# Kernel tuning notes

Hardware: AMD Instinct MI355X
Metric: run time of the kernel (lower is better)

The kernel has to match this reference:

```python
import jax, jax.numpy as jnp
import numpy as np

B, S, D, M = 2, 4096, 128, 64

def _linear_init(key, shape, fan_in):
    bound = 1.0 / np.sqrt(fan_in)
    return jax.random.uniform(key, shape, jnp.float32, -bound, bound)

def setup_inputs() -> dict:
    key = jax.random.key(0)
    ks = jax.random.split(key, 18)
    x = jax.random.normal(ks[0], (B, S, D), jnp.float32)
    context = jax.random.normal(ks[1], (B, S, D), jnp.float32)
    # per-mechanism params (torch Linear semantics: y = x @ W.T + b)
    Wt = _linear_init(ks[2], (M, D, D), D)   # transform weight, laid out [m, in, out]
    bt = _linear_init(ks[3], (M, D), D)
    char = jax.random.normal(ks[4], (M, D), jnp.float32)  # characteristics [1,1,d] per mech
    Wg = _linear_init(ks[5], (M, D), D)      # timing_gate weight (out=1)
    bg = _linear_init(ks[6], (M,), D)
    Wv = _linear_init(ks[7], (M, D), D)      # victory_detector weight (out=1)
    bv = _linear_init(ks[8], (M,), D)
    O = jax.random.normal(ks[9], (M, M), jnp.float32) * 0.02  # overcoming matrix
    # selector: Linear(2D,2D) -> GELU -> Linear(2D,M)
    W1 = _linear_init(ks[10], (2 * D, 2 * D), 2 * D)
    b1 = _linear_init(ks[11], (2 * D,), 2 * D)
    W2 = _linear_init(ks[12], (2 * D, M), 2 * D)
    b2 = _linear_init(ks[13], (M,), 2 * D)
    # integrate: Linear(2D, D)
    Wi = _linear_init(ks[14], (2 * D, D), 2 * D)
    bi = _linear_init(ks[15], (D,), 2 * D)
    return {"x": x, "context": context, "Wt": Wt, "bt": bt, "char": char,
            "Wg": Wg, "bg": bg, "Wv": Wv, "bv": bv, "O": O,
            "W1": W1, "b1": b1, "W2": W2, "b2": b2, "Wi": Wi, "bi": bi}

def reference(x, context, Wt, bt, char, Wg, bg, Wv, bv, O, W1, b1, W2, b2, Wi, bi):
    # selection scores over mechanisms
    sel_in = jnp.concatenate([x, context], axis=-1)          # [b,s,2d]
    h = jax.nn.gelu(sel_in @ W1 + b1, approximate=False)
    selection_scores = jax.nn.softmax(h @ W2 + b2, axis=-1)  # [b,s,m]
    # all 64 mechanism nodes as one batched GEMM
    transformed = jnp.einsum('bsd,mde->bsme', x, Wt) + bt + char   # [b,s,m,d]
    timing = jax.nn.sigmoid(jnp.einsum('bsd,md->bsm', x, Wg) + bg)  # [b,s,m]
    victory = jax.nn.sigmoid(jnp.einsum('bsme,me->bsm', transformed, Wv) + bv)
    outputs = transformed * timing[..., None]                # [b,s,m,d]
    # strategic overcoming modulation: gate = 1 + tanh(scores @ O)
    gates = 1.0 + jnp.tanh(selection_scores @ O)             # [b,s,m]
    selected = jnp.einsum('bsme,bsm->bse', outputs, gates * selection_scores)
    victory_potential = jnp.sum(victory * selection_scores, axis=-1)  # [b,s]
    integrated = jnp.concatenate([x, selected], axis=-1) @ Wi + bi    # [b,s,d]
    return integrated, victory_potential
```

## Files before the change

kernel.cpp:

```cpp
#include <hip/hip_runtime.h>
#include <hip/hip_bf16.h>


typedef __bf16 bf16_t;
typedef __bf16 bf16x8 __attribute__((ext_vector_type(8)));
typedef float  f32x4  __attribute__((ext_vector_type(4)));

#define WS_WTT      0u
#define WS_W1T      2097152u
#define WS_W2T      2228224u
#define WS_OT       2260992u
#define WS_WG       2269184u
#define WS_U        2285568u
#define WS_CVEC     2301952u
#define WS_BCT      2302208u
#define WS_WIT      2318592u
#define WS_W        2384128u
#define WS_SBIAS    4481280u
#define WS_SEL      8675584u

#define VP_OFF 1048576

__device__ __forceinline__ f32x4 mfma16(bf16x8 a, bf16x8 b, f32x4 c) {
  return __builtin_amdgcn_mfma_f32_16x16x32_bf16(a, b, c, 0, 0, 0);
}

__device__ __forceinline__ float gelu_exact(float v) {
  return 0.5f * v * (1.0f + erff(v * 0.70710678118654752f));
}
__device__ __forceinline__ float sigmoidf_(float v) {
  return 1.0f / (1.0f + __expf(-v));
}

__device__ __forceinline__ bf16x8 cvt8(float4 v0, float4 v1) {
  bf16x8 a;
  a[0] = (bf16_t)v0.x; a[1] = (bf16_t)v0.y; a[2] = (bf16_t)v0.z; a[3] = (bf16_t)v0.w;
  a[4] = (bf16_t)v1.x; a[5] = (bf16_t)v1.y; a[6] = (bf16_t)v1.z; a[7] = (bf16_t)v1.w;
  return a;
}

__global__ __launch_bounds__(256) void kprep(
    const float* __restrict__ Wt, const float* __restrict__ bt,
    const float* __restrict__ ch, const float* __restrict__ Wg,
    const float* __restrict__ Wv, const float* __restrict__ bv,
    const float* __restrict__ O, const float* __restrict__ W1,
    const float* __restrict__ W2, const float* __restrict__ Wi,
    char* __restrict__ ws)
{
  const int bid = blockIdx.x, tid = threadIdx.x;
  if (bid < 128) {
    const int m = bid >> 1, half = bid & 1;
    const float* wtm = Wt + m * 16384;
    bf16_t* wtt = (bf16_t*)(ws + WS_WTT) + m * 16384;
    const int ks = half * 2 + (tid >> 7), e = tid & 127;
    bf16_t tmp[32];
    #pragma unroll
    for (int dd = 0; dd < 32; ++dd)
      tmp[dd] = (bf16_t)wtm[(ks * 32 + dd) * 128 + e];
    bf16_t* dst = wtt + ks * 4096 + e * 32;
    #pragma unroll
    for (int g = 0; g < 4; ++g)
      *(bf16x8*)(dst + g * 8) = *(const bf16x8*)(tmp + g * 8);
    if (half == 0) {
      if (tid < 128) {
        const float* wvm = Wv + m * 128;
        float s = 0.f;
        for (int e2 = 0; e2 < 128; ++e2) s += wtm[tid * 128 + e2] * wvm[e2];
        ((bf16_t*)(ws + WS_U))[m * 128 + tid] = (bf16_t)s;
      } else if (tid == 128) {
        const float* wvm = Wv + m * 128;
        float s = bv[m];
        for (int e2 = 0; e2 < 128; ++e2) s += (bt[m * 128 + e2] + ch[m * 128 + e2]) * wvm[e2];
        ((float*)(ws + WS_CVEC))[m] = s;
      }
    }
  } else if (bid < 144) {
    int base = (bid - 128) * 256 + tid;
    int k = base >> 4, c0 = (base & 15) * 16;
    bf16_t* o = (bf16_t*)(ws + WS_W1T);
    #pragma unroll
    for (int j = 0; j < 16; ++j) o[(c0 + j) * 256 + k] = (bf16_t)W1[k * 256 + c0 + j];
  } else if (bid < 146) {
    int base = (bid - 144) * 256 + tid;
    int k = base >> 1, c0 = (base & 1) * 32;
    bf16_t* o = (bf16_t*)(ws + WS_W2T);
    #pragma unroll
    for (int j = 0; j < 32; ++j) o[(c0 + j) * 256 + k] = (bf16_t)W2[k * 64 + c0 + j];
  } else if (bid == 146) {
    int k = tid >> 2, c0 = (tid & 3) * 16;
    bf16_t* o = (bf16_t*)(ws + WS_OT);
    #pragma unroll
    for (int j = 0; j < 16; ++j) o[(c0 + j) * 64 + k] = (bf16_t)O[k * 64 + c0 + j];
  } else if (bid == 147) {
    bf16_t* o = (bf16_t*)(ws + WS_WG);
    #pragma unroll
    for (int j = 0; j < 32; ++j) o[tid * 32 + j] = (bf16_t)Wg[tid * 32 + j];
  } else if (bid == 148) {
    bf16_t* o = (bf16_t*)(ws + WS_BCT);
    #pragma unroll
    for (int i = 0; i < 4; ++i) {
      int task = tid + i * 256;
      int m = task >> 4, e0 = (task & 15) * 8;
      #pragma unroll
      for (int j = 0; j < 8; ++j)
        o[(e0 + j) * 64 + m] = (bf16_t)(bt[m * 128 + e0 + j] + ch[m * 128 + e0 + j]);
    }
  } else {
    int base = (bid - 149) * 256 + tid;
    int k = base >> 2, c0 = (base & 3) * 32;
    bf16_t* o = (bf16_t*)(ws + WS_WIT);
    #pragma unroll
    for (int j = 0; j < 32; ++j) o[(c0 + j) * 256 + k] = (bf16_t)Wi[k * 128 + c0 + j];
  }
}

__global__ __launch_bounds__(256) void kselect(
    const float* __restrict__ x, const float* __restrict__ ctx,
    const float* __restrict__ b1, const float* __restrict__ b2,
    const float* __restrict__ bg,
    char* __restrict__ ws, float* __restrict__ out)
{
  __shared__ char sm[41472];
  bf16_t* hL      = (bf16_t*)sm;
  float*  logitsL = (float*)(sm + 16384);
  float*  scoresL = (float*)(sm + 24576);
  bf16_t* scbL    = (bf16_t*)(sm + 32768);
  bf16_t* wbL     = (bf16_t*)(sm + 36864);
  float*  vpL     = (float*)(sm + 40960);

  const int tid = threadIdx.x;
  const int lane = tid & 63, wid = tid >> 6;
  const int tb = blockIdx.x * 32;
  const int lr = lane & 15;
  const int lk = (lane >> 4) * 8;
  const int lj4 = (lane >> 4) * 4;

  const bf16_t* W1t = (const bf16_t*)(ws + WS_W1T);
  const bf16_t* W2t = (const bf16_t*)(ws + WS_W2T);
  const bf16_t* Ot  = (const bf16_t*)(ws + WS_OT);
  const bf16_t* Wgb = (const bf16_t*)(ws + WS_WG);
  const bf16_t* Ub  = (const bf16_t*)(ws + WS_U);
  const float*  cv  = (const float*)(ws + WS_CVEC);
  const bf16_t* bct = (const bf16_t*)(ws + WS_BCT);
  float* wOut  = (float*)(ws + WS_W);
  float* sbOut = (float*)(ws + WS_SBIAS);

  bf16x8 aSel[2][8];
  #pragma unroll
  for (int rg = 0; rg < 2; ++rg) {
    int t = tb + rg * 16 + lr;
    #pragma unroll
    for (int ks = 0; ks < 8; ++ks) {
      const float* src = (ks < 4) ? (x + t * 128 + ks * 32 + lk)
                                  : (ctx + t * 128 + (ks - 4) * 32 + lk);
      aSel[rg][ks] = cvt8(*(const float4*)src, *(const float4*)(src + 4));
    }
  }

  #pragma unroll
  for (int cg = 0; cg < 4; ++cg) {
    int c = wid * 64 + cg * 16 + lr;
    f32x4 a0 = {0.f,0.f,0.f,0.f}, a1 = {0.f,0.f,0.f,0.f};
    #pragma unroll
    for (int ks = 0; ks < 8; ++ks) {
      bf16x8 b = *(const bf16x8*)(W1t + c * 256 + ks * 32 + lk);
      a0 = mfma16(aSel[0][ks], b, a0);
      a1 = mfma16(aSel[1][ks], b, a1);
    }
    float bb = b1[c];
    #pragma unroll
    for (int j = 0; j < 4; ++j) {
      int r0 = lj4 + j, r1 = 16 + lj4 + j;
      float v0 = gelu_exact(a0[j] + bb);
      float v1 = gelu_exact(a1[j] + bb);
      *(bf16_t*)((char*)hL + ((r0 * 512 + c * 2) ^ ((r0 & 7) << 4))) = (bf16_t)v0;
      *(bf16_t*)((char*)hL + ((r1 * 512 + c * 2) ^ ((r1 & 7) << 4))) = (bf16_t)v1;
    }
  }
  __syncthreads();

  {
    int c = wid * 16 + lr;
    f32x4 l0 = {0.f,0.f,0.f,0.f}, l1 = {0.f,0.f,0.f,0.f};
    #pragma unroll
    for (int ks = 0; ks < 8; ++ks) {
      int k0 = ks * 32 + lk;
      bf16x8 a0 = *(const bf16x8*)((char*)hL + ((lr * 512 + k0 * 2) ^ ((lr & 7) << 4)));
      bf16x8 a1 = *(const bf16x8*)((char*)hL + (((16 + lr) * 512 + k0 * 2) ^ ((lr & 7) << 4)));
      bf16x8 b  = *(const bf16x8*)(W2t + c * 256 + k0);
      l0 = mfma16(a0, b, l0);
      l1 = mfma16(a1, b, l1);
    }
    float bb = b2[c];
    #pragma unroll
    for (int j = 0; j < 4; ++j) {
      logitsL[(lj4 + j) * 64 + c] = l0[j] + bb;
      logitsL[(16 + lj4 + j) * 64 + c] = l1[j] + bb;
    }
  }
  __syncthreads();

  {
    int row = tid >> 3, i = tid & 7;
    float v[8];
    #pragma unroll
    for (int j = 0; j < 8; ++j) v[j] = logitsL[row * 64 + i * 8 + j];
    float mx = v[0];
    #pragma unroll
    for (int j = 1; j < 8; ++j) mx = fmaxf(mx, v[j]);
    mx = fmaxf(mx, __shfl_xor(mx, 1));
    mx = fmaxf(mx, __shfl_xor(mx, 2));
    mx = fmaxf(mx, __shfl_xor(mx, 4));
    float sum = 0.f;
    #pragma unroll
    for (int j = 0; j < 8; ++j) { v[j] = __expf(v[j] - mx); sum += v[j]; }
    sum += __shfl_xor(sum, 1);
    sum += __shfl_xor(sum, 2);
    sum += __shfl_xor(sum, 4);
    float inv = 1.0f / sum;
    #pragma unroll
    for (int j = 0; j < 8; ++j) {
      float s = v[j] * inv;
      int cc = i * 8 + j;
      scoresL[row * 64 + cc] = s;
      *(bf16_t*)((char*)scbL + ((row * 128 + cc * 2) ^ ((row & 7) << 4))) = (bf16_t)s;
    }
  }
  __syncthreads();

  const int c = wid * 16 + lr;
  f32x4 g0 = {0.f,0.f,0.f,0.f}, g1 = {0.f,0.f,0.f,0.f};
  #pragma unroll
  for (int ks = 0; ks < 2; ++ks) {
    int k0 = ks * 32 + lk;
    bf16x8 a0 = *(const bf16x8*)((char*)scbL + ((lr * 128 + k0 * 2) ^ ((lr & 7) << 4)));
    bf16x8 a1 = *(const bf16x8*)((char*)scbL + (((16 + lr) * 128 + k0 * 2) ^ ((lr & 7) << 4)));
    bf16x8 b  = *(const bf16x8*)(Ot + c * 64 + k0);
    g0 = mfma16(a0, b, g0);
    g1 = mfma16(a1, b, g1);
  }
  f32x4 t0 = {0.f,0.f,0.f,0.f}, t1 = {0.f,0.f,0.f,0.f};
  f32x4 v0 = {0.f,0.f,0.f,0.f}, v1 = {0.f,0.f,0.f,0.f};
  #pragma unroll
  for (int ks = 0; ks < 4; ++ks) {
    bf16x8 bT = *(const bf16x8*)(Wgb + c * 128 + ks * 32 + lk);
    bf16x8 bV = *(const bf16x8*)(Ub  + c * 128 + ks * 32 + lk);
    t0 = mfma16(aSel[0][ks], bT, t0);
    t1 = mfma16(aSel[1][ks], bT, t1);
    v0 = mfma16(aSel[0][ks], bV, v0);
    v1 = mfma16(aSel[1][ks], bV, v1);
  }
  {
    float bgc = bg[c], cvc = cv[c];
    #pragma unroll
    for (int j = 0; j < 4; ++j) {
      {
        int r = lj4 + j;
        float gate = 1.0f + tanhf(g0[j]);
        float tim  = sigmoidf_(t0[j] + bgc);
        float vic  = sigmoidf_(v0[j] + cvc);
        float sc   = scoresL[r * 64 + c];
        float w    = gate * sc * tim;
        wOut[(tb + r) * 64 + c] = w;
        *(bf16_t*)((char*)wbL + ((r * 128 + c * 2) ^ ((r & 7) << 4))) = (bf16_t)w;
        float pv = vic * sc;
        pv += __shfl_xor(pv, 1); pv += __shfl_xor(pv, 2);
        pv += __shfl_xor(pv, 4); pv += __shfl_xor(pv, 8);
        if (lr == 0) vpL[r * 4 + wid] = pv;
      }
      {
        int r = 16 + lj4 + j;
        float gate = 1.0f + tanhf(g1[j]);
        float tim  = sigmoidf_(t1[j] + bgc);
        float vic  = sigmoidf_(v1[j] + cvc);
        float sc   = scoresL[r * 64 + c];
        float w    = gate * sc * tim;
        wOut[(tb + r) * 64 + c] = w;
        *(bf16_t*)((char*)wbL + ((r * 128 + c * 2) ^ ((r & 7) << 4))) = (bf16_t)w;
        float pv = vic * sc;
        pv += __shfl_xor(pv, 1); pv += __shfl_xor(pv, 2);
        pv += __shfl_xor(pv, 4); pv += __shfl_xor(pv, 8);
        if (lr == 0) vpL[r * 4 + wid] = pv;
      }
    }
  }
  __syncthreads();

  {
    f32x4 s00 = {0.f,0.f,0.f,0.f}, s01 = {0.f,0.f,0.f,0.f};
    f32x4 s10 = {0.f,0.f,0.f,0.f}, s11 = {0.f,0.f,0.f,0.f};
    int c0 = wid * 32 + lr, c1 = wid * 32 + 16 + lr;
    #pragma unroll
    for (int ks = 0; ks < 2; ++ks) {
      int k0 = ks * 32 + lk;
      bf16x8 a0 = *(const bf16x8*)((char*)wbL + ((lr * 128 + k0 * 2) ^ ((lr & 7) << 4)));
      bf16x8 a1 = *(const bf16x8*)((char*)wbL + (((16 + lr) * 128 + k0 * 2) ^ ((lr & 7) << 4)));
      bf16x8 bb0 = *(const bf16x8*)(bct + c0 * 64 + k0);
      bf16x8 bb1 = *(const bf16x8*)(bct + c1 * 64 + k0);
      s00 = mfma16(a0, bb0, s00); s01 = mfma16(a0, bb1, s01);
      s10 = mfma16(a1, bb0, s10); s11 = mfma16(a1, bb1, s11);
    }
    #pragma unroll
    for (int j = 0; j < 4; ++j) {
      sbOut[(tb + lj4 + j) * 128 + c0] = s00[j];
      sbOut[(tb + lj4 + j) * 128 + c1] = s01[j];
      sbOut[(tb + 16 + lj4 + j) * 128 + c0] = s10[j];
      sbOut[(tb + 16 + lj4 + j) * 128 + c1] = s11[j];
    }
  }
  if (tid < 32) {
    float s = vpL[tid * 4 + 0] + vpL[tid * 4 + 1] + vpL[tid * 4 + 2] + vpL[tid * 4 + 3];
    out[VP_OFF + tb + tid] = s;
  }
}

__device__ __forceinline__ void loadF(bf16x8 (&F)[4], const char* bbase, int m) {
  const char* p = bbase + m * 32768;
  F[0] = *(const bf16x8*)(p);
  F[1] = *(const bf16x8*)(p + 8192);
  F[2] = *(const bf16x8*)(p + 16384);
  F[3] = *(const bf16x8*)(p + 24576);
}

template<int J>
__device__ __forceinline__ void computeT(const bf16x8 (&F)[4], const f32x4 (&wc)[16],
                                         const bf16x8 (&aX)[4][4], f32x4 (&acc)[4]) {
  #pragma unroll
  for (int rg = 0; rg < 4; ++rg) {
    f32x4 y = {0.f, 0.f, 0.f, 0.f};
    #pragma unroll
    for (int ks = 0; ks < 4; ++ks) y = mfma16(aX[rg][ks], F[ks], y);
    #pragma unroll
    for (int jj = 0; jj < 4; ++jj)
      acc[rg][jj] += wc[rg * 4 + jj][J] * y[jj];
  }
}

__global__ __launch_bounds__(256, 1) void kmech(
    const float* __restrict__ x, char* __restrict__ ws)
{
  __shared__ float wL[64 * 64];
  const int tid = threadIdx.x;
  const int lane = tid & 63, wid = tid >> 6;
  const int tb = (blockIdx.x >> 1) * 64;
  const int eh = blockIdx.x & 1;
  const int lr = lane & 15, lg = lane >> 4;
  const int lj4 = lg * 4;
  const int wcol = wid * 16;

  const char* wttc = (const char*)(ws + WS_WTT);
  const float* wIn  = (const float*)(ws + WS_W);
  const float* sbIn = (const float*)(ws + WS_SBIAS);
  float* selOut = (float*)(ws + WS_SEL);

  {
    const float4* s = (const float4*)(wIn + tb * 64);
    float4* d = (float4*)wL;
    #pragma unroll
    for (int i = 0; i < 4; ++i) d[tid + i * 256] = s[tid + i * 256];
  }
  bf16x8 aX[4][4];
  #pragma unroll
  for (int rg = 0; rg < 4; ++rg) {
    const float* xr = x + (tb + rg * 16 + lr) * 128;
    #pragma unroll
    for (int ks = 0; ks < 4; ++ks)
      aX[rg][ks] = cvt8(*(const float4*)(xr + ks * 32 + lg * 8),
                        *(const float4*)(xr + ks * 32 + lg * 8 + 4));
  }
  f32x4 acc[4];
  #pragma unroll
  for (int rg = 0; rg < 4; ++rg) {
    f32x4 a;
    #pragma unroll
    for (int j = 0; j < 4; ++j)
      a[j] = sbIn[(tb + rg * 16 + lj4 + j) * 128 + eh * 64 + wcol + lr];
    acc[rg] = a;
  }
  __syncthreads();

  const char* bbase = wttc + (size_t)(((eh * 64 + wcol + lr) * 32 + lg * 8) * 2);

  bf16x8 F0[4], F1[4], F2[4], F3[4];
  loadF(F0, bbase, 0);
  loadF(F1, bbase, 1);
  loadF(F2, bbase, 2);

  for (int it = 0; it < 16; ++it) {
    const int base = it * 4;
    f32x4 wc[16];
    #pragma unroll
    for (int rg = 0; rg < 4; ++rg)
      #pragma unroll
      for (int jj = 0; jj < 4; ++jj)
        wc[rg * 4 + jj] = *(const f32x4*)(&wL[(rg * 16 + lj4 + jj) * 64 + base]);
    int n3 = base + 3;
    int n4 = base + 4 > 63 ? 63 : base + 4;
    int n5 = base + 5 > 63 ? 63 : base + 5;
    int n6 = base + 6 > 63 ? 63 : base + 6;
    loadF(F3, bbase, n3);
    computeT<0>(F0, wc, aX, acc);
    loadF(F0, bbase, n4);
    computeT<1>(F1, wc, aX, acc);
    loadF(F1, bbase, n5);
    computeT<2>(F2, wc, aX, acc);
    loadF(F2, bbase, n6);
    computeT<3>(F3, wc, aX, acc);
  }

  #pragma unroll
  for (int rg = 0; rg < 4; ++rg)
    #pragma unroll
    for (int j = 0; j < 4; ++j)
      selOut[(tb + rg * 16 + lj4 + j) * 128 + eh * 64 + wcol + lr] = acc[rg][j];
}

__global__ __launch_bounds__(256) void kinteg(
    const float* __restrict__ x, const float* __restrict__ bi,
    const char* __restrict__ ws, float* __restrict__ out)
{
  const int tid = threadIdx.x;
  const int lane = tid & 63, wid = tid >> 6;
  const int tb = blockIdx.x * 32;
  const int lr = lane & 15, lk = (lane >> 4) * 8, lj4 = (lane >> 4) * 4;
  const bf16_t* Wit = (const bf16_t*)(ws + WS_WIT);
  const float* sel = (const float*)(ws + WS_SEL);

  bf16x8 aF[2][8];
  #pragma unroll
  for (int rg = 0; rg < 2; ++rg) {
    int t = tb + rg * 16 + lr;
    #pragma unroll
    for (int ks = 0; ks < 8; ++ks) {
      const float* src = (ks < 4) ? (x + t * 128 + ks * 32 + lk)
                                  : (sel + t * 128 + (ks - 4) * 32 + lk);
      aF[rg][ks] = cvt8(*(const float4*)src, *(const float4*)(src + 4));
    }
  }
  #pragma unroll
  for (int cg = 0; cg < 2; ++cg) {
    int c = wid * 32 + cg * 16 + lr;
    f32x4 a0 = {0.f,0.f,0.f,0.f}, a1 = {0.f,0.f,0.f,0.f};
    #pragma unroll
    for (int ks = 0; ks < 8; ++ks) {
      bf16x8 b = *(const bf16x8*)(Wit + c * 256 + ks * 32 + lk);
      a0 = mfma16(aF[0][ks], b, a0);
      a1 = mfma16(aF[1][ks], b, a1);
    }
    float bb = bi[c];
    #pragma unroll
    for (int j = 0; j < 4; ++j) {
      out[(tb + lj4 + j) * 128 + c] = a0[j] + bb;
      out[(tb + 16 + lj4 + j) * 128 + c] = a1[j] + bb;
    }
  }
}

extern "C" void kernel_launch(void* const* d_in, const int* in_sizes, int n_in,
                              void* d_out, int out_size, void* d_ws, size_t ws_size,
                              hipStream_t stream)
{
  (void)in_sizes; (void)n_in; (void)out_size; (void)ws_size;
  const float* x   = (const float*)d_in[0];
  const float* ctx = (const float*)d_in[1];
  const float* Wt  = (const float*)d_in[2];
  const float* bt  = (const float*)d_in[3];
  const float* ch  = (const float*)d_in[4];
  const float* Wg  = (const float*)d_in[5];
  const float* bg  = (const float*)d_in[6];
  const float* Wv  = (const float*)d_in[7];
  const float* bv  = (const float*)d_in[8];
  const float* O   = (const float*)d_in[9];
  const float* W1  = (const float*)d_in[10];
  const float* b1  = (const float*)d_in[11];
  const float* W2  = (const float*)d_in[12];
  const float* b2  = (const float*)d_in[13];
  const float* Wi  = (const float*)d_in[14];
  const float* bi  = (const float*)d_in[15];
  float* out = (float*)d_out;
  char* ws = (char*)d_ws;

  kprep<<<153, 256, 0, stream>>>(Wt, bt, ch, Wg, Wv, bv, O, W1, W2, Wi, ws);
  kselect<<<256, 256, 0, stream>>>(x, ctx, b1, b2, bg, ws, out);
  kmech<<<256, 256, 0, stream>>>(x, ws);
  kinteg<<<256, 256, 0, stream>>>(x, bi, ws, out);
}
```

Measured before the change: 143.8 us.

## Fuse select, mechanism and integrate kernels into one per-tile kernel

Merges the selector, mechanism-GEMM and integration kernels into a single kernel that processes 64-token tiles split across two blocks by output half. The gating weights, selected vector and bias terms stay in shared memory instead of round-tripping through workspace global memory, and two kernel launches are removed. Each of the two half-blocks now recomputes the full selector MLP, which duplicates that work. The partial integration results are combined with atomicAdd into the output, so a memset is required before launch.

```diff
diff --git a/kernel.cpp b/kernel.cpp
--- a/kernel.cpp
+++ b/kernel.cpp
@@ -15,9 +15,6 @@
 #define WS_CVEC     2301952u
 #define WS_BCT      2302208u
 #define WS_WIT      2318592u
-#define WS_W        2384128u
-#define WS_SBIAS    4481280u
-#define WS_SEL      8675584u
 
 #define VP_OFF 1048576
 
@@ -114,26 +111,51 @@
   }
 }
 
-__global__ __launch_bounds__(256) void kselect(
+__device__ __forceinline__ void loadF(bf16x8 (&F)[4], const char* bbase, int m) {
+  const char* p = bbase + m * 32768;
+  F[0] = *(const bf16x8*)(p);
+  F[1] = *(const bf16x8*)(p + 8192);
+  F[2] = *(const bf16x8*)(p + 16384);
+  F[3] = *(const bf16x8*)(p + 24576);
+}
+
+template<int J>
+__device__ __forceinline__ void computeT(const bf16x8 (&F)[4], const f32x4 (&wc)[16],
+                                         const bf16x8 (&aSel)[4][8], f32x4 (&acc)[4]) {
+  #pragma unroll
+  for (int rg = 0; rg < 4; ++rg) {
+    f32x4 y = {0.f, 0.f, 0.f, 0.f};
+    #pragma unroll
+    for (int ks = 0; ks < 4; ++ks) y = mfma16(aSel[rg][ks], F[ks], y);
+    #pragma unroll
+    for (int jj = 0; jj < 4; ++jj)
+      acc[rg][jj] += wc[rg * 4 + jj][J] * y[jj];
+  }
+}
+
+__global__ __launch_bounds__(256, 1) void kfused(
     const float* __restrict__ x, const float* __restrict__ ctx,
     const float* __restrict__ b1, const float* __restrict__ b2,
-    const float* __restrict__ bg,
+    const float* __restrict__ bg, const float* __restrict__ bi,
     char* __restrict__ ws, float* __restrict__ out)
 {
-  __shared__ char sm[41472];
+  __shared__ char sm[92160];
   bf16_t* hL      = (bf16_t*)sm;
-  float*  logitsL = (float*)(sm + 16384);
-  float*  scoresL = (float*)(sm + 24576);
-  bf16_t* scbL    = (bf16_t*)(sm + 32768);
-  bf16_t* wbL     = (bf16_t*)(sm + 36864);
-  float*  vpL     = (float*)(sm + 40960);
+  float*  scoresL = (float*)(sm + 32768);
+  float*  wL      = (float*)(sm + 49152);
+  bf16_t* scbL    = (bf16_t*)(sm + 66560);
+  bf16_t* wbL     = (bf16_t*)(sm + 74752);
+  bf16_t* selL    = (bf16_t*)(sm + 82944);
+  float*  vpL     = (float*)(sm + 91136);
 
   const int tid = threadIdx.x;
   const int lane = tid & 63, wid = tid >> 6;
-  const int tb = blockIdx.x * 32;
+  const int tb = (blockIdx.x >> 1) * 64;
+  const int eh = blockIdx.x & 1;
   const int lr = lane & 15;
-  const int lk = (lane >> 4) * 8;
-  const int lj4 = (lane >> 4) * 4;
+  const int lg = lane >> 4;
+  const int lk = lg * 8;
+  const int lj4 = lg * 4;
 
   const bf16_t* W1t = (const bf16_t*)(ws + WS_W1T);
   const bf16_t* W2t = (const bf16_t*)(ws + WS_W2T);
@@ -142,12 +164,12 @@
   const bf16_t* Ub  = (const bf16_t*)(ws + WS_U);
   const float*  cv  = (const float*)(ws + WS_CVEC);
   const bf16_t* bct = (const bf16_t*)(ws + WS_BCT);
-  float* wOut  = (float*)(ws + WS_W);
-  float* sbOut = (float*)(ws + WS_SBIAS);
-
-  bf16x8 aSel[2][8];
+  const bf16_t* Wit = (const bf16_t*)(ws + WS_WIT);
+  const char*  wttc = (const char*)(ws + WS_WTT);
+
+  bf16x8 aSel[4][8];
   #pragma unroll
-  for (int rg = 0; rg < 2; ++rg) {
+  for (int rg = 0; rg < 4; ++rg) {
     int t = tb + rg * 16 + lr;
     #pragma unroll
     for (int ks = 0; ks < 8; ++ks) {
@@ -160,227 +182,144 @@
   #pragma unroll
   for (int cg = 0; cg < 4; ++cg) {
     int c = wid * 64 + cg * 16 + lr;
-    f32x4 a0 = {0.f,0.f,0.f,0.f}, a1 = {0.f,0.f,0.f,0.f};
+    f32x4 a[4] = {{0,0,0,0},{0,0,0,0},{0,0,0,0},{0,0,0,0}};
     #pragma unroll
     for (int ks = 0; ks < 8; ++ks) {
       bf16x8 b = *(const bf16x8*)(W1t + c * 256 + ks * 32 + lk);
-      a0 = mfma16(aSel[0][ks], b, a0);
-      a1 = mfma16(aSel[1][ks], b, a1);
+      #pragma unroll
+      for (int rg = 0; rg < 4; ++rg) a[rg] = mfma16(aSel[rg][ks], b, a[rg]);
     }
     float bb = b1[c];
     #pragma unroll
-    for (int j = 0; j < 4; ++j) {
-      int r0 = lj4 + j, r1 = 16 + lj4 + j;
-      float v0 = gelu_exact(a0[j] + bb);
-      float v1 = gelu_exact(a1[j] + bb);
-      *(bf16_t*)((char*)hL + ((r0 * 512 + c * 2) ^ ((r0 & 7) << 4))) = (bf16_t)v0;
-      *(bf16_t*)((char*)hL + ((r1 * 512 + c * 2) ^ ((r1 & 7) << 4))) = (bf16_t)v1;
-    }
+    for (int rg = 0; rg < 4; ++rg)
+      #pragma unroll
+      for (int j = 0; j < 4; ++j) {
+        int r = rg * 16 + lj4 + j;
+        float v = gelu_exact(a[rg][j] + bb);
+        *(bf16_t*)((char*)hL + ((r * 512 + c * 2) ^ ((r & 7) << 4))) = (bf16_t)v;
+      }
   }
   __syncthreads();
 
   {
     int c = wid * 16 + lr;
-    f32x4 l0 = {0.f,0.f,0.f,0.f}, l1 = {0.f,0.f,0.f,0.f};
+    f32x4 l[4] = {{0,0,0,0},{0,0,0,0},{0,0,0,0},{0,0,0,0}};
     #pragma unroll
     for (int ks = 0; ks < 8; ++ks) {
       int k0 = ks * 32 + lk;
-      bf16x8 a0 = *(const bf16x8*)((char*)hL + ((lr * 512 + k0 * 2) ^ ((lr & 7) << 4)));
-      bf16x8 a1 = *(const bf16x8*)((char*)hL + (((16 + lr) * 512 + k0 * 2) ^ ((lr & 7) << 4)));
-      bf16x8 b  = *(const bf16x8*)(W2t + c * 256 + k0);
-      l0 = mfma16(a0, b, l0);
-      l1 = mfma16(a1, b, l1);
+      bf16x8 b = *(const bf16x8*)(W2t + c * 256 + k0);
+      #pragma unroll
+      for (int rg = 0; rg < 4; ++rg) {
+        int r = rg * 16 + lr;
+        bf16x8 a = *(const bf16x8*)((char*)hL + ((r * 512 + k0 * 2) ^ ((r & 7) << 4)));
+        l[rg] = mfma16(a, b, l[rg]);
+      }
     }
     float bb = b2[c];
     #pragma unroll
-    for (int j = 0; j < 4; ++j) {
-      logitsL[(lj4 + j) * 64 + c] = l0[j] + bb;
-      logitsL[(16 + lj4 + j) * 64 + c] = l1[j] + bb;
-    }
+    for (int rg = 0; rg < 4; ++rg)
+      #pragma unroll
+      for (int j = 0; j < 4; ++j)
+        scoresL[(rg * 16 + lj4 + j) * 64 + c] = l[rg][j] + bb;
   }
   __syncthreads();
 
   {
-    int row = tid >> 3, i = tid & 7;
-    float v[8];
-    #pragma unroll
-    for (int j = 0; j < 8; ++j) v[j] = logitsL[row * 64 + i * 8 + j];
+    int row = tid >> 2, i = tid & 3;
+    float v[16];
+    #pragma unroll
+    for (int j = 0; j < 16; ++j) v[j] = scoresL[row * 64 + i * 16 + j];
     float mx = v[0];
     #pragma unroll
-    for (int j = 1; j < 8; ++j) mx = fmaxf(mx, v[j]);
+    for (int j = 1; j < 16; ++j) mx = fmaxf(mx, v[j]);
     mx = fmaxf(mx, __shfl_xor(mx, 1));
     mx = fmaxf(mx, __shfl_xor(mx, 2));
-    mx = fmaxf(mx, __shfl_xor(mx, 4));
     float sum = 0.f;
     #pragma unroll
-    for (int j = 0; j < 8; ++j) { v[j] = __expf(v[j] - mx); sum += v[j]; }
+    for (int j = 0; j < 16; ++j) { v[j] = __expf(v[j] - mx); sum += v[j]; }
     sum += __shfl_xor(sum, 1);
     sum += __shfl_xor(sum, 2);
-    sum += __shfl_xor(sum, 4);
     float inv = 1.0f / sum;
     #pragma unroll
-    for (int j = 0; j < 8; ++j) {
+    for (int j = 0; j < 16; ++j) {
       float s = v[j] * inv;
-      int cc = i * 8 + j;
+      int cc = i * 16 + j;
       scoresL[row * 64 + cc] = s;
       *(bf16_t*)((char*)scbL + ((row * 128 + cc * 2) ^ ((row & 7) << 4))) = (bf16_t)s;
     }
   }
   __syncthreads();
 
-  const int c = wid * 16 + lr;
-  f32x4 g0 = {0.f,0.f,0.f,0.f}, g1 = {0.f,0.f,0.f,0.f};
-  #pragma unroll
-  for (int ks = 0; ks < 2; ++ks) {
-    int k0 = ks * 32 + lk;
-    bf16x8 a0 = *(const bf16x8*)((char*)scbL + ((lr * 128 + k0 * 2) ^ ((lr & 7) << 4)));
-    bf16x8 a1 = *(const bf16x8*)((char*)scbL + (((16 + lr) * 128 + k0 * 2) ^ ((lr & 7) << 4)));
-    bf16x8 b  = *(const bf16x8*)(Ot + c * 64 + k0);
-    g0 = mfma16(a0, b, g0);
-    g1 = mfma16(a1, b, g1);
-  }
-  f32x4 t0 = {0.f,0.f,0.f,0.f}, t1 = {0.f,0.f,0.f,0.f};
-  f32x4 v0 = {0.f,0.f,0.f,0.f}, v1 = {0.f,0.f,0.f,0.f};
-  #pragma unroll
-  for (int ks = 0; ks < 4; ++ks) {
-    bf16x8 bT = *(const bf16x8*)(Wgb + c * 128 + ks * 32 + lk);
-    bf16x8 bV = *(const bf16x8*)(Ub  + c * 128 + ks * 32 + lk);
-    t0 = mfma16(aSel[0][ks], bT, t0);
-    t1 = mfma16(aSel[1][ks], bT, t1);
-    v0 = mfma16(aSel[0][ks], bV, v0);
-    v1 = mfma16(aSel[1][ks], bV, v1);
-  }
   {
+    const int c = wid * 16 + lr;
+    f32x4 g[4] = {{0,0,0,0},{0,0,0,0},{0,0,0,0},{0,0,0,0}};
+    #pragma unroll
+    for (int ks = 0; ks < 2; ++ks) {
+      int k0 = ks * 32 + lk;
+      bf16x8 b = *(const bf16x8*)(Ot + c * 64 + k0);
+      #pragma unroll
+      for (int rg = 0; rg < 4; ++rg) {
+        int r = rg * 16 + lr;
+        bf16x8 a = *(const bf16x8*)((char*)scbL + ((r * 128 + k0 * 2) ^ ((r & 7) << 4)));
+        g[rg] = mfma16(a, b, g[rg]);
+      }
+    }
+    f32x4 t[4] = {{0,0,0,0},{0,0,0,0},{0,0,0,0},{0,0,0,0}};
+    f32x4 v[4] = {{0,0,0,0},{0,0,0,0},{0,0,0,0},{0,0,0,0}};
+    #pragma unroll
+    for (int ks = 0; ks < 4; ++ks) {
+      bf16x8 bT = *(const bf16x8*)(Wgb + c * 128 + ks * 32 + lk);
+      bf16x8 bV = *(const bf16x8*)(Ub  + c * 128 + ks * 32 + lk);
+      #pragma unroll
+      for (int rg = 0; rg < 4; ++rg) {
+        t[rg] = mfma16(aSel[rg][ks], bT, t[rg]);
+        v[rg] = mfma16(aSel[rg][ks], bV, v[rg]);
+      }
+    }
     float bgc = bg[c], cvc = cv[c];
     #pragma unroll
-    for (int j = 0; j < 4; ++j) {
-      {
-        int r = lj4 + j;
-        float gate = 1.0f + tanhf(g0[j]);
-        float tim  = sigmoidf_(t0[j] + bgc);
-        float vic  = sigmoidf_(v0[j] + cvc);
+    for (int rg = 0; rg < 4; ++rg)
+      #pragma unroll
+      for (int j = 0; j < 4; ++j) {
+        int r = rg * 16 + lj4 + j;
+        float gate = 1.0f + tanhf(g[rg][j]);
+        float tim  = sigmoidf_(t[rg][j] + bgc);
+        float vic  = sigmoidf_(v[rg][j] + cvc);
         float sc   = scoresL[r * 64 + c];
         float w    = gate * sc * tim;
-        wOut[(tb + r) * 64 + c] = w;
+        wL[r * 68 + c] = w;
         *(bf16_t*)((char*)wbL + ((r * 128 + c * 2) ^ ((r & 7) << 4))) = (bf16_t)w;
         float pv = vic * sc;
         pv += __shfl_xor(pv, 1); pv += __shfl_xor(pv, 2);
         pv += __shfl_xor(pv, 4); pv += __shfl_xor(pv, 8);
         if (lr == 0) vpL[r * 4 + wid] = pv;
       }
-      {
-        int r = 16 + lj4 + j;
-        float gate = 1.0f + tanhf(g1[j]);
-        float tim  = sigmoidf_(t1[j] + bgc);
-        float vic  = sigmoidf_(v1[j] + cvc);
-        float sc   = scoresL[r * 64 + c];
-        float w    = gate * sc * tim;
-        wOut[(tb + r) * 64 + c] = w;
-        *(bf16_t*)((char*)wbL + ((r * 128 + c * 2) ^ ((r & 7) << 4))) = (bf16_t)w;
-        float pv = vic * sc;
-        pv += __shfl_xor(pv, 1); pv += __shfl_xor(pv, 2);
-        pv += __shfl_xor(pv, 4); pv += __shfl_xor(pv, 8);
-        if (lr == 0) vpL[r * 4 + wid] = pv;
-      }
-    }
   }
   __syncthreads();
 
+  if (eh == 0 && tid < 64) {
+    float s = vpL[tid * 4 + 0] + vpL[tid * 4 + 1] + vpL[tid * 4 + 2] + vpL[tid * 4 + 3];
+    out[VP_OFF + tb + tid] = s;
+  }
+
+  const int wcol = wid * 16;
+  f32x4 acc[4] = {{0,0,0,0},{0,0,0,0},{0,0,0,0},{0,0,0,0}};
   {
-    f32x4 s00 = {0.f,0.f,0.f,0.f}, s01 = {0.f,0.f,0.f,0.f};
-    f32x4 s10 = {0.f,0.f,0.f,0.f}, s11 = {0.f,0.f,0.f,0.f};
-    int c0 = wid * 32 + lr, c1 = wid * 32 + 16 + lr;
+    int eg = eh * 64 + wcol + lr;
     #pragma unroll
     for (int ks = 0; ks < 2; ++ks) {
       int k0 = ks * 32 + lk;
-      bf16x8 a0 = *(const bf16x8*)((char*)wbL + ((lr * 128 + k0 * 2) ^ ((lr & 7) << 4)));
-      bf16x8 a1 = *(const bf16x8*)((char*)wbL + (((16 + lr) * 128 + k0 * 2) ^ ((lr & 7) << 4)));
-      bf16x8 bb0 = *(const bf16x8*)(bct + c0 * 64 + k0);
-      bf16x8 bb1 = *(const bf16x8*)(bct + c1 * 64 + k0);
-      s00 = mfma16(a0, bb0, s00); s01 = mfma16(a0, bb1, s01);
-      s10 = mfma16(a1, bb0, s10); s11 = mfma16(a1, bb1, s11);
-    }
-    #pragma unroll
-    for (int j = 0; j < 4; ++j) {
-      sbOut[(tb + lj4 + j) * 128 + c0] = s00[j];
-      sbOut[(tb + lj4 + j) * 128 + c1] = s01[j];
-      sbOut[(tb + 16 + lj4 + j) * 128 + c0] = s10[j];
-      sbOut[(tb + 16 + lj4 + j) * 128 + c1] = s11[j];
-    }
-  }
-  if (tid < 32) {
-    float s = vpL[tid * 4 + 0] + vpL[tid * 4 + 1] + vpL[tid * 4 + 2] + vpL[tid * 4 + 3];
-    out[VP_OFF + tb + tid] = s;
-  }
-}
-
-__device__ __forceinline__ void loadF(bf16x8 (&F)[4], const char* bbase, int m) {
-  const char* p = bbase + m * 32768;
-  F[0] = *(const bf16x8*)(p);
-  F[1] = *(const bf16x8*)(p + 8192);
-  F[2] = *(const bf16x8*)(p + 16384);
-  F[3] = *(const bf16x8*)(p + 24576);
-}
-
-template<int J>
-__device__ __forceinline__ void computeT(const bf16x8 (&F)[4], const f32x4 (&wc)[16],
-                                         const bf16x8 (&aX)[4][4], f32x4 (&acc)[4]) {
-  #pragma unroll
-  for (int rg = 0; rg < 4; ++rg) {
-    f32x4 y = {0.f, 0.f, 0.f, 0.f};
-    #pragma unroll
-    for (int ks = 0; ks < 4; ++ks) y = mfma16(aX[rg][ks], F[ks], y);
-    #pragma unroll
-    for (int jj = 0; jj < 4; ++jj)
-      acc[rg][jj] += wc[rg * 4 + jj][J] * y[jj];
-  }
-}
-
-__global__ __launch_bounds__(256, 1) void kmech(
-    const float* __restrict__ x, char* __restrict__ ws)
-{
-  __shared__ float wL[64 * 64];
-  const int tid = threadIdx.x;
-  const int lane = tid & 63, wid = tid >> 6;
-  const int tb = (blockIdx.x >> 1) * 64;
-  const int eh = blockIdx.x & 1;
-  const int lr = lane & 15, lg = lane >> 4;
-  const int lj4 = lg * 4;
-  const int wcol = wid * 16;
-
-  const char* wttc = (const char*)(ws + WS_WTT);
-  const float* wIn  = (const float*)(ws + WS_W);
-  const float* sbIn = (const float*)(ws + WS_SBIAS);
-  float* selOut = (float*)(ws + WS_SEL);
-
-  {
-    const float4* s = (const float4*)(wIn + tb * 64);
-    float4* d = (float4*)wL;
-    #pragma unroll
-    for (int i = 0; i < 4; ++i) d[tid + i * 256] = s[tid + i * 256];
-  }
-  bf16x8 aX[4][4];
-  #pragma unroll
-  for (int rg = 0; rg < 4; ++rg) {
-    const float* xr = x + (tb + rg * 16 + lr) * 128;
-    #pragma unroll
-    for (int ks = 0; ks < 4; ++ks)
-      aX[rg][ks] = cvt8(*(const float4*)(xr + ks * 32 + lg * 8),
-                        *(const float4*)(xr + ks * 32 + lg * 8 + 4));
-  }
-  f32x4 acc[4];
-  #pragma unroll
-  for (int rg = 0; rg < 4; ++rg) {
-    f32x4 a;
-    #pragma unroll
-    for (int j = 0; j < 4; ++j)
-      a[j] = sbIn[(tb + rg * 16 + lj4 + j) * 128 + eh * 64 + wcol + lr];
-    acc[rg] = a;
-  }
-  __syncthreads();
+      bf16x8 b = *(const bf16x8*)(bct + eg * 64 + k0);
+      #pragma unroll
+      for (int rg = 0; rg < 4; ++rg) {
+        int r = rg * 16 + lr;
+        bf16x8 a = *(const bf16x8*)((char*)wbL + ((r * 128 + k0 * 2) ^ ((r & 7) << 4)));
+        acc[rg] = mfma16(a, b, acc[rg]);
+      }
+    }
+  }
 
   const char* bbase = wttc + (size_t)(((eh * 64 + wcol + lr) * 32 + lg * 8) * 2);
-
   bf16x8 F0[4], F1[4], F2[4], F3[4];
   loadF(F0, bbase, 0);
   loadF(F1, bbase, 1);
@@ -393,66 +332,59 @@
     for (int rg = 0; rg < 4; ++rg)
       #pragma unroll
       for (int jj = 0; jj < 4; ++jj)
-        wc[rg * 4 + jj] = *(const f32x4*)(&wL[(rg * 16 + lj4 + jj) * 64 + base]);
-    int n3 = base + 3;
+        wc[rg * 4 + jj] = *(const f32x4*)(&wL[(rg * 16 + lj4 + jj) * 68 + base]);
     int n4 = base + 4 > 63 ? 63 : base + 4;
     int n5 = base + 5 > 63 ? 63 : base + 5;
     int n6 = base + 6 > 63 ? 63 : base + 6;
-    loadF(F3, bbase, n3);
-    computeT<0>(F0, wc, aX, acc);
+    loadF(F3, bbase, base + 3);
+    computeT<0>(F0, wc, aSel, acc);
     loadF(F0, bbase, n4);
-    computeT<1>(F1, wc, aX, acc);
+    computeT<1>(F1, wc, aSel, acc);
     loadF(F1, bbase, n5);
-    computeT<2>(F2, wc, aX, acc);
+    computeT<2>(F2, wc, aSel, acc);
     loadF(F2, bbase, n6);
-    computeT<3>(F3, wc, aX, acc);
+    computeT<3>(F3, wc, aSel, acc);
   }
 
   #pragma unroll
   for (int rg = 0; rg < 4; ++rg)
     #pragma unroll
-    for (int j = 0; j < 4; ++j)
-      selOut[(tb + rg * 16 + lj4 + j) * 128 + eh * 64 + wcol + lr] = acc[rg][j];
-}
-
-__global__ __launch_bounds__(256) void kinteg(
-    const float* __restrict__ x, const float* __restrict__ bi,
-    const char* __restrict__ ws, float* __restrict__ out)
-{
-  const int tid = threadIdx.x;
-  const int lane = tid & 63, wid = tid >> 6;
-  const int tb = blockIdx.x * 32;
-  const int lr = lane & 15, lk = (lane >> 4) * 8, lj4 = (lane >> 4) * 4;
-  const bf16_t* Wit = (const bf16_t*)(ws + WS_WIT);
-  const float* sel = (const float*)(ws + WS_SEL);
-
-  bf16x8 aF[2][8];
-  #pragma unroll
-  for (int rg = 0; rg < 2; ++rg) {
-    int t = tb + rg * 16 + lr;
-    #pragma unroll
-    for (int ks = 0; ks < 8; ++ks) {
-      const float* src = (ks < 4) ? (x + t * 128 + ks * 32 + lk)
-                                  : (sel + t * 128 + (ks - 4) * 32 + lk);
-      aF[rg][ks] = cvt8(*(const float4*)src, *(const float4*)(src + 4));
-    }
-  }
+    for (int j = 0; j < 4; ++j) {
+      int r = rg * 16 + lj4 + j;
+      int cl = wcol + lr;
+      *(bf16_t*)((char*)selL + ((r * 128 + cl * 2) ^ ((r & 7) << 4))) = (bf16_t)acc[rg][j];
+    }
+  __syncthreads();
+
   #pragma unroll
   for (int cg = 0; cg < 2; ++cg) {
     int c = wid * 32 + cg * 16 + lr;
-    f32x4 a0 = {0.f,0.f,0.f,0.f}, a1 = {0.f,0.f,0.f,0.f};
-    #pragma unroll
-    for (int ks = 0; ks < 8; ++ks) {
-      bf16x8 b = *(const bf16x8*)(Wit + c * 256 + ks * 32 + lk);
-      a0 = mfma16(aF[0][ks], b, a0);
-      a1 = mfma16(aF[1][ks], b, a1);
-    }
-    float bb = bi[c];
-    #pragma unroll
-    for (int j = 0; j < 4; ++j) {
-      out[(tb + lj4 + j) * 128 + c] = a0[j] + bb;
-      out[(tb + 16 + lj4 + j) * 128 + c] = a1[j] + bb;
-    }
+    f32x4 a[4] = {{0,0,0,0},{0,0,0,0},{0,0,0,0},{0,0,0,0}};
+    #pragma unroll
+    for (int ks = 0; ks < 2; ++ks) {
+      int k0 = ks * 32 + lk;
+      bf16x8 b = *(const bf16x8*)(Wit + c * 256 + 128 + eh * 64 + k0);
+      #pragma unroll
+      for (int rg = 0; rg < 4; ++rg) {
+        int r = rg * 16 + lr;
+        bf16x8 av = *(const bf16x8*)((char*)selL + ((r * 128 + k0 * 2) ^ ((r & 7) << 4)));
+        a[rg] = mfma16(av, b, a[rg]);
+      }
+    }
+    if (eh == 0) {
+      #pragma unroll
+      for (int ks = 0; ks < 4; ++ks) {
+        bf16x8 b = *(const bf16x8*)(Wit + c * 256 + ks * 32 + lk);
+        #pragma unroll
+        for (int rg = 0; rg < 4; ++rg) a[rg] = mfma16(aSel[rg][ks], b, a[rg]);
+      }
+    }
+    float bb = (eh == 0) ? bi[c] : 0.0f;
+    #pragma unroll
+    for (int rg = 0; rg < 4; ++rg)
+      #pragma unroll
+      for (int j = 0; j < 4; ++j)
+        atomicAdd(&out[(tb + rg * 16 + lj4 + j) * 128 + c], a[rg][j] + bb);
   }
 }
 
@@ -460,7 +392,7 @@
                               void* d_out, int out_size, void* d_ws, size_t ws_size,
                               hipStream_t stream)
 {
-  (void)in_sizes; (void)n_in; (void)out_size; (void)ws_size;
+  (void)in_sizes; (void)n_in; (void)ws_size;
   const float* x   = (const float*)d_in[0];
   const float* ctx = (const float*)d_in[1];
   const float* Wt  = (const float*)d_in[2];
@@ -480,8 +412,7 @@
   float* out = (float*)d_out;
   char* ws = (char*)d_ws;
 
+  hipMemsetAsync(d_out, 0, (size_t)out_size * 4, stream);
   kprep<<<153, 256, 0, stream>>>(Wt, bt, ch, Wg, Wv, bv, O, W1, W2, Wi, ws);
-  kselect<<<256, 256, 0, stream>>>(x, ctx, b1, b2, bg, ws, out);
-  kmech<<<256, 256, 0, stream>>>(x, ws);
-  kinteg<<<256, 256, 0, stream>>>(x, bi, ws, out);
-}
+  kfused<<<256, 256, 0, stream>>>(x, ctx, b1, b2, bg, bi, ws, out);
+}
```

Result: slower. 146.8 us (+2.1%).
